# Kernel tuning notes

Hardware: AMD Instinct MI355X
Metric: run time of the kernel (lower is better)

The kernel has to match this reference:

```python
import jax, jax.numpy as jnp
import numpy as np

# ---- StatDenoiser constants (init: spatial_radius=3, temporal_radius=1, alpha=0.005, spp=32) ----
SPATIAL_RADIUS = 3
TEMPORAL_RADIUS = 1
KS = 2 * SPATIAL_RADIUS + 1          # 7
KT = 2 * TEMPORAL_RADIUS + 1         # 3
N_PATCHES = KS * KS * KT             # 147
CENTER = N_PATCHES // 2              # 73 == rs*(KS*KT) + rs*KT + rt (odd sizes)
GAMMA_W = 2.907                      # scipy.stats.t.ppf(1 - 0.005/2, 32+32-2) precomputed
SIGMA_INV = jnp.asarray([0.1, 0.1, 0.1, 50.0, 50.0, 50.0, 10.0, 10.0, 10.0],
                        dtype=jnp.float32).reshape(-1, 1, 1, 1, 1)  # (9,1,1,1,1)


def shift(x):
    """Neighbors of every pixel with zero padding. x:(C,H,W,T) -> (C,P,H,W,T).
    Patch ordering (dh, dw, dt) matches torch unfold(1).unfold(2).unfold(3)."""
    C, H, W, T = x.shape
    xp = jnp.pad(x, ((0, 0), (SPATIAL_RADIUS,) * 2, (SPATIAL_RADIUS,) * 2, (TEMPORAL_RADIUS,) * 2))
    patches = [xp[:, i:i + H, j:j + W, k:k + T]
               for i in range(KS) for j in range(KS) for k in range(KT)]
    return jnp.stack(patches, axis=1)


def _compute_w(ei, ej, vi, vj):
    """Optimal weight w_ij between pixel i (center) and neighbor j."""
    d2 = (ei - ej) ** 2
    num = 2.0 * d2 + vi + vj
    den = 2.0 * (d2 + vi + vj)
    res = num / jnp.where(den == 0, 1.0, den)
    res = jnp.where((num == 0) & (den == 0), 0.5, res)
    res = jnp.where(((vi == 0) | (vj == 0)) & (ei != ej), 1.0, res)
    return res


def setup_inputs() -> dict:
    key = jax.random.key(0)
    k1, k2, k3, k4 = jax.random.split(key, 4)
    H, W, T = 64, 64, 16
    image = jax.random.uniform(k1, (3, H, W, T), dtype=jnp.float32)
    guidance = jax.random.uniform(k2, (9, H, W, T), dtype=jnp.float32)
    estimands = jax.random.uniform(k3, (3, H, W, T), dtype=jnp.float32)
    estimands_variance = jax.random.uniform(k4, (3, H, W, T), dtype=jnp.float32) * 0.01
    return {"image": image, "guidance": guidance,
            "estimands": estimands, "estimands_variance": estimands_variance}


def reference(image, guidance, estimands, estimands_variance):
    # Bilateral (range) weights from the guidance buffers.
    sg = shift(guidance)                                  # (9,P,H,W,T)
    diff2 = (sg - sg[:, CENTER:CENTER + 1]) ** 2
    bilateral = jnp.exp(-0.5 * jnp.sum(diff2 * SIGMA_INV, axis=0))   # (P,H,W,T)

    # Statistical-test membership (Welch-style t-test on estimand means/variances).
    se = shift(estimands)                                 # (3,P,H,W,T)
    sv = shift(estimands_variance)
    w_ij = _compute_w(se[:, CENTER:CENTER + 1], se,
                      sv[:, CENTER:CENTER + 1], sv)       # (3,P,H,W,T)
    arg = jnp.maximum(1.0 / (2.0 * (1.0 - w_ij)) - 1.0, 0.0)
    t_stat = jnp.where(w_ij == 1.0, jnp.inf, jnp.sqrt(arg))
    membership = jnp.all(t_stat < GAMMA_W, axis=0).astype(jnp.float32)  # (P,H,W,T)
    membership = membership.at[CENTER].set(1.0)

    # Combine: normalized (bilateral * membership) weighting of neighbor radiance.
    weights = bilateral * membership
    weights = weights / jnp.sum(weights, axis=0, keepdims=True)  # center weight==1 => sum>=1
    si = shift(image)                                      # (3,P,H,W,T)
    out = jnp.sum(si * weights[None], axis=1)              # (3,H,W,T)
    return out
```

## Files before the change

### kernel.cpp

```cpp
#include <hip/hip_runtime.h>

#define HH 64
#define WW 64
#define TT 16
#define NPIX (HH * WW * TT)

__global__ __launch_bounds__(512) void statdenoise_kernel(
    const float* __restrict__ img,
    const float* __restrict__ gui,
    const float* __restrict__ est,
    const float* __restrict__ var,
    float* __restrict__ out)
{
    const float SIG[9] = {0.1f, 0.1f, 0.1f, 50.0f, 50.0f, 50.0f, 10.0f, 10.0f, 10.0f};
    const float G2 = 2.907f * 2.907f;

    const int lane = threadIdx.x & 63;
    const int s    = threadIdx.x >> 6;
    const int tg   = lane & 7;
    const int hwl  = lane >> 3;
    const int hw   = blockIdx.x * 8 + hwl;
    const int h    = hw >> 6;
    const int w    = hw & 63;
    const int t0   = tg * 2;
    const int cpx  = hw * 16 + t0;

    float2 gc[9];
#pragma unroll
    for (int c = 0; c < 9; ++c) gc[c] = *(const float2*)&gui[c * NPIX + cpx];
    float2 ec[3], vc[3];
#pragma unroll
    for (int c = 0; c < 3; ++c) {
        ec[c] = *(const float2*)&est[c * NPIX + cpx];
        vc[c] = *(const float2*)&var[c * NPIX + cpx];
    }

    const bool vLo = (t0 != 0);
    const bool vHi = (t0 != 14);

    float acc[2][4] = {};

    int dh = s / 7 - 3;
    int dw = s % 7 - 3;
    for (int r = s; r < 49; r += 8) {
        const int hh = h + dh;
        if ((unsigned)hh < (unsigned)HH) {
            const int ww   = w + dw;
            const bool colOK = (unsigned)ww < (unsigned)WW;
            const int wwc  = colOK ? ww : (ww < 0 ? 0 : WW - 1);
            const int off0 = (((hh << 6) + wwc) << 4) + t0;

            float sb[2][3] = {};
#pragma unroll
            for (int c = 0; c < 9; ++c) {
                const float* g = gui + c * NPIX;
                float2 m = *(const float2*)&g[off0];
                float lo = __shfl_up(m.y, 1);
                float hi = __shfl_down(m.x, 1);
                float nv[4] = {lo, m.x, m.y, hi};
#pragma unroll
                for (int e = 0; e < 2; ++e) {
                    float ce = e ? gc[c].y : gc[c].x;
#pragma unroll
                    for (int k = 0; k < 3; ++k) {
                        float d = ce - nv[e + k];
                        sb[e][k] = fmaf(d * d, SIG[c], sb[e][k]);
                    }
                }
            }

            bool mem[2][3] = {{true, true, true}, {true, true, true}};
#pragma unroll
            for (int c = 0; c < 3; ++c) {
                const float* ep = est + c * NPIX;
                const float* vp = var + c * NPIX;
                float2 em = *(const float2*)&ep[off0];
                float2 vm = *(const float2*)&vp[off0];
                float env[4] = {__shfl_up(em.y, 1), em.x, em.y, __shfl_down(em.x, 1)};
                float vnv[4] = {__shfl_up(vm.y, 1), vm.x, vm.y, __shfl_down(vm.x, 1)};
#pragma unroll
                for (int e = 0; e < 2; ++e) {
                    float ece = e ? ec[c].y : ec[c].x;
                    float vce = e ? vc[c].y : vc[c].x;
#pragma unroll
                    for (int k = 0; k < 3; ++k) {
                        float d  = ece - env[e + k];
                        float d2 = d * d;
                        float V  = vce + vnv[e + k];
                        bool pass = (d2 < G2 * V) | ((d2 == 0.f) & (V == 0.f));
                        bool kill = ((vce == 0.f) | (vnv[e + k] == 0.f)) & (d2 != 0.f);
                        mem[e][k] = mem[e][k] & pass & (!kill);
                    }
                }
            }

            float wt[2][3];
#pragma unroll
            for (int e = 0; e < 2; ++e) {
#pragma unroll
                for (int k = 0; k < 3; ++k) {
                    bool ok = colOK;
                    if (e == 0 && k == 0) ok = ok && vLo;
                    if (e == 1 && k == 2) ok = ok && vHi;
                    float b = __expf(-0.5f * sb[e][k]);
                    wt[e][k] = (ok && mem[e][k]) ? b : 0.f;
                }
            }

#pragma unroll
            for (int c = 0; c < 3; ++c) {
                const float* ip = img + c * NPIX;
                float2 im = *(const float2*)&ip[off0];
                float inv[4] = {__shfl_up(im.y, 1), im.x, im.y, __shfl_down(im.x, 1)};
#pragma unroll
                for (int e = 0; e < 2; ++e) {
                    float a = 0.f;
#pragma unroll
                    for (int k = 0; k < 3; ++k) a = fmaf(wt[e][k], inv[e + k], a);
                    acc[e][c] += a;
                }
            }
#pragma unroll
            for (int e = 0; e < 2; ++e)
                acc[e][3] += wt[e][0] + wt[e][1] + wt[e][2];
        }
        dw += 8;
        while (dw > 3) { dw -= 7; ++dh; }
    }

    __shared__ float4 red[2][8][64];
    red[0][s][lane] = make_float4(acc[0][0], acc[0][1], acc[0][2], acc[0][3]);
    red[1][s][lane] = make_float4(acc[1][0], acc[1][1], acc[1][2], acc[1][3]);
    __syncthreads();

    if (threadIdx.x < 128) {
        const int j = threadIdx.x;
        const int l = j >> 1, e = j & 1;
        float4 sum = red[e][0][l];
#pragma unroll
        for (int q = 1; q < 8; ++q) {
            float4 v = red[e][q][l];
            sum.x += v.x; sum.y += v.y; sum.z += v.z; sum.w += v.w;
        }
        const int px = blockIdx.x * 128 + j;
        const float inv = 1.f / sum.w;
        out[0 * NPIX + px] = sum.x * inv;
        out[1 * NPIX + px] = sum.y * inv;
        out[2 * NPIX + px] = sum.z * inv;
    }
}

extern "C" void kernel_launch(void* const* d_in, const int* in_sizes, int n_in,
                              void* d_out, int out_size, void* d_ws, size_t ws_size,
                              hipStream_t stream) {
    const float* img = (const float*)d_in[0];
    const float* gui = (const float*)d_in[1];
    const float* est = (const float*)d_in[2];
    const float* var = (const float*)d_in[3];
    float* out = (float*)d_out;

    dim3 grid(4096 / 8);
    dim3 block(512);
    statdenoise_kernel<<<grid, block, 0, stream>>>(img, gui, est, var, out);
}
```

Baseline: 28.88 us.

## Use one temporal pixel per thread with DPP neighbor exchange and double grid

After: 71.76 us. +148.5%, slower.

```diff
diff --git a/kernel.cpp b/kernel.cpp
--- a/kernel.cpp
+++ b/kernel.cpp
@@ -5,7 +5,16 @@
 #define TT 16
 #define NPIX (HH * WW * TT)
 
-__global__ __launch_bounds__(512) void statdenoise_kernel(
+__device__ __forceinline__ float dpp_up1(float x) {
+    return __int_as_float(__builtin_amdgcn_update_dpp(
+        0, __float_as_int(x), 0x111, 0xF, 0xF, true));
+}
+__device__ __forceinline__ float dpp_dn1(float x) {
+    return __int_as_float(__builtin_amdgcn_update_dpp(
+        0, __float_as_int(x), 0x101, 0xF, 0xF, true));
+}
+
+__global__ __launch_bounds__(512, 8) void statdenoise_kernel(
     const float* __restrict__ img,
     const float* __restrict__ gui,
     const float* __restrict__ est,
@@ -17,132 +26,100 @@
 
     const int lane = threadIdx.x & 63;
     const int s    = threadIdx.x >> 6;
-    const int tg   = lane & 7;
-    const int hwl  = lane >> 3;
-    const int hw   = blockIdx.x * 8 + hwl;
+    const int tg   = lane & 15;
+    const int hwl  = lane >> 4;
+    const int hw   = blockIdx.x * 4 + hwl;
     const int h    = hw >> 6;
     const int w    = hw & 63;
-    const int t0   = tg * 2;
-    const int cpx  = hw * 16 + t0;
+    const int cpx  = hw * 16 + tg;
 
-    float2 gc[9];
+    float gc[9];
 #pragma unroll
-    for (int c = 0; c < 9; ++c) gc[c] = *(const float2*)&gui[c * NPIX + cpx];
-    float2 ec[3], vc[3];
+    for (int c = 0; c < 9; ++c) gc[c] = gui[c * NPIX + cpx];
+    float ec[3], vc[3];
 #pragma unroll
     for (int c = 0; c < 3; ++c) {
-        ec[c] = *(const float2*)&est[c * NPIX + cpx];
-        vc[c] = *(const float2*)&var[c * NPIX + cpx];
+        ec[c] = est[c * NPIX + cpx];
+        vc[c] = var[c * NPIX + cpx];
     }
 
-    const bool vLo = (t0 != 0);
-    const bool vHi = (t0 != 14);
+    const bool vLo = (tg > 0);
+    const bool vHi = (tg < 15);
 
-    float acc[2][4] = {};
+    float acc[4] = {0.f, 0.f, 0.f, 0.f};
 
-    int dh = s / 7 - 3;
-    int dw = s % 7 - 3;
+    int dh = s / 7 - 3, dw = s % 7 - 3;
     for (int r = s; r < 49; r += 8) {
         const int hh = h + dh;
         if ((unsigned)hh < (unsigned)HH) {
             const int ww   = w + dw;
             const bool colOK = (unsigned)ww < (unsigned)WW;
             const int wwc  = colOK ? ww : (ww < 0 ? 0 : WW - 1);
-            const int off0 = (((hh << 6) + wwc) << 4) + t0;
+            const int off0 = (((hh << 6) + wwc) << 4) + tg;
 
-            float sb[2][3] = {};
+            float sb[3] = {0.f, 0.f, 0.f};
 #pragma unroll
             for (int c = 0; c < 9; ++c) {
-                const float* g = gui + c * NPIX;
-                float2 m = *(const float2*)&g[off0];
-                float lo = __shfl_up(m.y, 1);
-                float hi = __shfl_down(m.x, 1);
-                float nv[4] = {lo, m.x, m.y, hi};
+                float m = gui[c * NPIX + off0];
+                float nv[3] = {dpp_up1(m), m, dpp_dn1(m)};
 #pragma unroll
-                for (int e = 0; e < 2; ++e) {
-                    float ce = e ? gc[c].y : gc[c].x;
-#pragma unroll
-                    for (int k = 0; k < 3; ++k) {
-                        float d = ce - nv[e + k];
-                        sb[e][k] = fmaf(d * d, SIG[c], sb[e][k]);
-                    }
+                for (int k = 0; k < 3; ++k) {
+                    float d = gc[c] - nv[k];
+                    sb[k] = fmaf(d * d, SIG[c], sb[k]);
                 }
             }
 
-            bool mem[2][3] = {{true, true, true}, {true, true, true}};
+            bool mem[3] = {true, true, true};
 #pragma unroll
             for (int c = 0; c < 3; ++c) {
-                const float* ep = est + c * NPIX;
-                const float* vp = var + c * NPIX;
-                float2 em = *(const float2*)&ep[off0];
-                float2 vm = *(const float2*)&vp[off0];
-                float env[4] = {__shfl_up(em.y, 1), em.x, em.y, __shfl_down(em.x, 1)};
-                float vnv[4] = {__shfl_up(vm.y, 1), vm.x, vm.y, __shfl_down(vm.x, 1)};
+                float em = est[c * NPIX + off0];
+                float vm = var[c * NPIX + off0];
+                float env[3] = {dpp_up1(em), em, dpp_dn1(em)};
+                float vnv[3] = {dpp_up1(vm), vm, dpp_dn1(vm)};
 #pragma unroll
-                for (int e = 0; e < 2; ++e) {
-                    float ece = e ? ec[c].y : ec[c].x;
-                    float vce = e ? vc[c].y : vc[c].x;
-#pragma unroll
-                    for (int k = 0; k < 3; ++k) {
-                        float d  = ece - env[e + k];
-                        float d2 = d * d;
-                        float V  = vce + vnv[e + k];
-                        bool pass = (d2 < G2 * V) | ((d2 == 0.f) & (V == 0.f));
-                        bool kill = ((vce == 0.f) | (vnv[e + k] == 0.f)) & (d2 != 0.f);
-                        mem[e][k] = mem[e][k] & pass & (!kill);
-                    }
+                for (int k = 0; k < 3; ++k) {
+                    float d  = ec[c] - env[k];
+                    float d2 = d * d;
+                    float V  = vc[c] + vnv[k];
+                    bool pass = (d2 < G2 * V) | ((d2 == 0.f) & (V == 0.f));
+                    bool kill = ((vc[c] == 0.f) | (vnv[k] == 0.f)) & (d2 != 0.f);
+                    mem[k] = mem[k] & pass & (!kill);
                 }
             }
 
-            float wt[2][3];
+            float wt[3];
 #pragma unroll
-            for (int e = 0; e < 2; ++e) {
-#pragma unroll
-                for (int k = 0; k < 3; ++k) {
-                    bool ok = colOK;
-                    if (e == 0 && k == 0) ok = ok && vLo;
-                    if (e == 1 && k == 2) ok = ok && vHi;
-                    float b = __expf(-0.5f * sb[e][k]);
-                    wt[e][k] = (ok && mem[e][k]) ? b : 0.f;
-                }
+            for (int k = 0; k < 3; ++k) {
+                bool ok = colOK && mem[k];
+                if (k == 0) ok = ok && vLo;
+                if (k == 2) ok = ok && vHi;
+                wt[k] = ok ? __expf(-0.5f * sb[k]) : 0.f;
             }
 
 #pragma unroll
             for (int c = 0; c < 3; ++c) {
-                const float* ip = img + c * NPIX;
-                float2 im = *(const float2*)&ip[off0];
-                float inv[4] = {__shfl_up(im.y, 1), im.x, im.y, __shfl_down(im.x, 1)};
-#pragma unroll
-                for (int e = 0; e < 2; ++e) {
-                    float a = 0.f;
-#pragma unroll
-                    for (int k = 0; k < 3; ++k) a = fmaf(wt[e][k], inv[e + k], a);
-                    acc[e][c] += a;
-                }
+                float im = img[c * NPIX + off0];
+                float iv[3] = {dpp_up1(im), im, dpp_dn1(im)};
+                acc[c] = fmaf(wt[0], iv[0], fmaf(wt[1], iv[1], fmaf(wt[2], iv[2], acc[c])));
             }
-#pragma unroll
-            for (int e = 0; e < 2; ++e)
-                acc[e][3] += wt[e][0] + wt[e][1] + wt[e][2];
+            acc[3] += wt[0] + wt[1] + wt[2];
         }
         dw += 8;
         while (dw > 3) { dw -= 7; ++dh; }
     }
 
-    __shared__ float4 red[2][8][64];
-    red[0][s][lane] = make_float4(acc[0][0], acc[0][1], acc[0][2], acc[0][3]);
-    red[1][s][lane] = make_float4(acc[1][0], acc[1][1], acc[1][2], acc[1][3]);
+    __shared__ float4 red[8][64];
+    red[s][lane] = make_float4(acc[0], acc[1], acc[2], acc[3]);
     __syncthreads();
 
-    if (threadIdx.x < 128) {
-        const int j = threadIdx.x;
-        const int l = j >> 1, e = j & 1;
-        float4 sum = red[e][0][l];
+    if (threadIdx.x < 64) {
+        float4 sum = red[0][lane];
 #pragma unroll
         for (int q = 1; q < 8; ++q) {
-            float4 v = red[e][q][l];
+            float4 v = red[q][lane];
             sum.x += v.x; sum.y += v.y; sum.z += v.z; sum.w += v.w;
         }
-        const int px = blockIdx.x * 128 + j;
+        const int px = blockIdx.x * 64 + lane;
         const float inv = 1.f / sum.w;
         out[0 * NPIX + px] = sum.x * inv;
         out[1 * NPIX + px] = sum.y * inv;
@@ -159,7 +136,7 @@
     const float* var = (const float*)d_in[3];
     float* out = (float*)d_out;
 
-    dim3 grid(4096 / 8);
+    dim3 grid(4096 / 4);
     dim3 block(512);
     statdenoise_kernel<<<grid, block, 0, stream>>>(img, gui, est, var, out);
 }
```
